# Optimization experiments

Measured on AMD Instinct MI355X. Metric: run time of the kernel, lower is better.

## Reference

```python
import jax, jax.numpy as jnp
import numpy as np

N_TOK = 131072
N_EMB = 1024
EMB_DIM = 64
COMMIT = 0.25


def setup_inputs() -> dict:
    key = jax.random.key(0)
    k1, k2 = jax.random.split(key)
    z_e = jax.random.normal(k1, (N_TOK, EMB_DIM), dtype=jnp.float32)
    # nn.init.uniform_(weight, -1/K, 1/K)
    codebook = jax.random.uniform(k2, (N_EMB, EMB_DIM), dtype=jnp.float32,
                                  minval=-1.0 / N_EMB, maxval=1.0 / N_EMB)
    return {"z_e": z_e, "codebook": codebook}


def reference(z_e, codebook):
    sg = jax.lax.stop_gradient
    # ||a-b||^2 = ||a||^2 + ||b||^2 - 2 a.b  (avoids [N,K,D] broadcast)
    d = (jnp.sum(z_e * z_e, axis=-1, keepdims=True)          # [N,1]
         + jnp.sum(codebook * codebook, axis=-1)[None, :]    # [1,K]
         - 2.0 * jnp.einsum('nd,kd->nk', z_e, codebook))     # [N,K]
    indices = jnp.argmin(d, axis=-1)                          # [N] int
    z_q = codebook[indices]                                   # [N,D] gather

    codebook_loss = jnp.mean((z_q - sg(z_e)) ** 2)
    commitment_loss = jnp.mean((z_e - sg(z_q)) ** 2)
    loss = codebook_loss + COMMIT * commitment_loss

    z_q_st = z_e + sg(z_q - z_e)                              # straight-through

    # avg_probs = one_hot(indices).mean(0) via scatter-add histogram
    counts = jnp.zeros((N_EMB,), dtype=jnp.float32).at[indices].add(1.0)
    avg_probs = counts / z_e.shape[0]
    perplexity = jnp.exp(-jnp.sum(avg_probs * jnp.log(avg_probs + 1e-10)))

    return z_q_st, loss, perplexity, indices
```

## Files before the change

### kernel.cpp

```cpp
#include <hip/hip_runtime.h>
#include <math.h>

#define NTOK 131072
#define NEMB 1024
#define DIM  64
#define OUT_LOSS (NTOK * DIM)
#define OUT_PERP (OUT_LOSS + 1)
#define OUT_IDX  (OUT_LOSS + 2)

#define EPS_FLAG 6e-5f

typedef short bf16x8 __attribute__((ext_vector_type(8)));
typedef float f32x4  __attribute__((ext_vector_type(4)));
typedef const __attribute__((address_space(1))) void* gas_t;
typedef __attribute__((address_space(3))) void* las_t;

__device__ __forceinline__ float sqb(float x) {
    float y = x * x;
    asm volatile("" : "+v"(y));
    return y;
}
#define NP_PAIRWISE_SQ64(GET, RES)                                     \
    do {                                                               \
        float r0 = sqb(GET(0)), r1 = sqb(GET(1)), r2 = sqb(GET(2)),    \
              r3 = sqb(GET(3)), r4 = sqb(GET(4)), r5 = sqb(GET(5)),    \
              r6 = sqb(GET(6)), r7 = sqb(GET(7));                      \
        _Pragma("unroll")                                              \
        for (int i = 8; i < 64; i += 8) {                              \
            r0 += sqb(GET(i + 0)); r1 += sqb(GET(i + 1));              \
            r2 += sqb(GET(i + 2)); r3 += sqb(GET(i + 3));              \
            r4 += sqb(GET(i + 4)); r5 += sqb(GET(i + 5));              \
            r6 += sqb(GET(i + 6)); r7 += sqb(GET(i + 7));              \
        }                                                              \
        RES = ((r0 + r1) + (r2 + r3)) + ((r4 + r5) + (r6 + r7));       \
    } while (0)

__device__ __forceinline__ unsigned short f2bf_rne(float x) {
    unsigned u = __float_as_uint(x);
    u += 0x7FFFu + ((u >> 16) & 1u);
    return (unsigned short)(u >> 16);
}
__device__ __forceinline__ float bf2f(unsigned short b) {
    return __uint_as_float(((unsigned)b) << 16);
}


__global__ void vq_prep(const float* __restrict__ cb, float* __restrict__ h,
                        unsigned short* __restrict__ ch, unsigned short* __restrict__ cl,
                        double* __restrict__ sse, int* __restrict__ counts,
                        int* __restrict__ done) {
    if (blockIdx.x == 0) {
        if (threadIdx.x == 0) { *sse = 0.0; *done = 0; }
        for (int i = threadIdx.x; i < NEMB * 16; i += 256) counts[i] = 0;
    }
    int k = blockIdx.x * 256 + threadIdx.x;
    if (k >= NEMB) return;
    float c[64];
    const float4* p = (const float4*)(cb + k * DIM);
#pragma unroll
    for (int q = 0; q < 16; ++q) {
        float4 v = p[q];
        c[4 * q] = v.x; c[4 * q + 1] = v.y; c[4 * q + 2] = v.z; c[4 * q + 3] = v.w;
    }
    float hk;
#define GETC(d) (c[d])
    NP_PAIRWISE_SQ64(GETC, hk);
#undef GETC
    h[k] = hk;
#pragma unroll
    for (int b = 0; b < 8; ++b) {
        unsigned uhv[4], ulv[4];
#pragma unroll
        for (int e = 0; e < 4; ++e) {
            float x0 = -2.0f * c[b * 8 + e * 2 + 0];
            float x1 = -2.0f * c[b * 8 + e * 2 + 1];
            unsigned short h0 = f2bf_rne(x0), h1 = f2bf_rne(x1);
            unsigned short l0 = f2bf_rne(x0 - bf2f(h0)), l1 = f2bf_rne(x1 - bf2f(h1));
            uhv[e] = (unsigned)h0 | ((unsigned)h1 << 16);
            ulv[e] = (unsigned)l0 | ((unsigned)l1 << 16);
        }
        *(uint4*)(ch + k * 64 + b * 8) = make_uint4(uhv[0], uhv[1], uhv[2], uhv[3]);
        *(uint4*)(cl + k * 64 + b * 8) = make_uint4(ulv[0], ulv[1], ulv[2], ulv[3]);
    }
}

__global__ __launch_bounds__(512) void vq_screen(
    const float*          __restrict__ ze,
    const float*          __restrict__ cb,
    const unsigned short* __restrict__ ch_g,
    const unsigned short* __restrict__ cl_g,
    const float*          __restrict__ h_g,
    float*                __restrict__ out,
    int*                  __restrict__ aux,
    double*               __restrict__ sse_g,
    int*                  __restrict__ counts) {
    __shared__ __align__(16) char lds[53376];
    const int tid  = threadIdx.x;
    const int lane = tid & 63;
    const int wid  = tid >> 6;
    const int col  = lane & 15;
    const int grp  = lane >> 4;
    const int tbase = blockIdx.x * 256 + wid * 32;

    const int srow = tid >> 3, scol = tid & 7;
    const int srcoff = (srow * 8 + (scol ^ (srow & 7))) * 16;

    bf16x8 zh[2][2], zl[2][2];
#pragma unroll
    for (int tt = 0; tt < 2; ++tt)
#pragma unroll
        for (int s = 0; s < 2; ++s) {
            const float* zp = ze + (size_t)(tbase + tt * 16 + col) * 64 + s * 32 + grp * 8;
            float4 v0 = *(const float4*)(zp);
            float4 v1 = *(const float4*)(zp + 4);
            float zv[8] = {v0.x, v0.y, v0.z, v0.w, v1.x, v1.y, v1.z, v1.w};
            bf16x8 hfr, lfr;
#pragma unroll
            for (int j = 0; j < 8; ++j) {
                unsigned short hb = f2bf_rne(zv[j]);
                unsigned short lb = f2bf_rne(zv[j] - bf2f(hb));
                hfr[j] = (short)hb;
                lfr[j] = (short)lb;
            }
            zh[tt][s] = hfr;
            zl[tt][s] = lfr;
        }

    float m1[2] = {INFINITY, INFINITY}, m2[2] = {INFINITY, INFINITY};
    float m3[2] = {INFINITY, INFINITY};
    int   ki[2] = {0, 0}, i2[2] = {0, 0};

#define STAGE(cc, b)                                                           \
    do {                                                                       \
        __builtin_amdgcn_global_load_lds(                                      \
            (gas_t)((const char*)ch_g + (cc) * 8192 + srcoff),                 \
            (las_t)(lds + (b) * 16384 + wid * 1024), 16, 0, 0);                \
        __builtin_amdgcn_global_load_lds(                                      \
            (gas_t)((const char*)cl_g + (cc) * 8192 + srcoff),                 \
            (las_t)(lds + (b) * 16384 + 8192 + wid * 1024), 16, 0, 0);         \
    } while (0)

#define TOP3UPD(tt, s, kk)                                                     \
    do {                                                                       \
        bool lt1 = (s) < m1[tt], lt2 = (s) < m2[tt], lt3 = (s) < m3[tt];       \
        m3[tt] = lt2 ? m2[tt] : (lt3 ? (s) : m3[tt]);                          \
        i2[tt] = lt1 ? ki[tt] : (lt2 ? (kk) : i2[tt]);                         \
        m2[tt] = lt1 ? m1[tt] : (lt2 ? (s) : m2[tt]);                          \
        ki[tt] = lt1 ? (kk) : ki[tt];                                          \
        m1[tt] = lt1 ? (s) : m1[tt];                                           \
    } while (0)

#define COMPUTE(cc, b)                                                         \
    do {                                                                       \
        _Pragma("unroll")                                                      \
        for (int ct = 0; ct < 4; ++ct) {                                       \
            const int arow = (b) * 16384 + ct * 2048 + col * 128;              \
            bf16x8 ach0 = *(const bf16x8*)(lds + arow + ((((0 * 4) + grp) ^ (col & 7)) << 4)); \
            bf16x8 ach1 = *(const bf16x8*)(lds + arow + ((((1 * 4) + grp) ^ (col & 7)) << 4)); \
            bf16x8 acl0 = *(const bf16x8*)(lds + arow + 8192 + ((((0 * 4) + grp) ^ (col & 7)) << 4)); \
            bf16x8 acl1 = *(const bf16x8*)(lds + arow + 8192 + ((((1 * 4) + grp) ^ (col & 7)) << 4)); \
            f32x4 hv = *(const f32x4*)(lds + 49152 + (cc) * 256 + ct * 64 + grp * 16); \
            f32x4 acc0 = hv, acc1 = hv;                                        \
            acc0 = __builtin_amdgcn_mfma_f32_16x16x32_bf16(ach0, zh[0][0], acc0, 0, 0, 0); \
            acc1 = __builtin_amdgcn_mfma_f32_16x16x32_bf16(ach0, zh[1][0], acc1, 0, 0, 0); \
            acc0 = __builtin_amdgcn_mfma_f32_16x16x32_bf16(ach1, zh[0][1], acc0, 0, 0, 0); \
            acc1 = __builtin_amdgcn_mfma_f32_16x16x32_bf16(ach1, zh[1][1], acc1, 0, 0, 0); \
            acc0 = __builtin_amdgcn_mfma_f32_16x16x32_bf16(ach0, zl[0][0], acc0, 0, 0, 0); \
            acc1 = __builtin_amdgcn_mfma_f32_16x16x32_bf16(ach0, zl[1][0], acc1, 0, 0, 0); \
            acc0 = __builtin_amdgcn_mfma_f32_16x16x32_bf16(ach1, zl[0][1], acc0, 0, 0, 0); \
            acc1 = __builtin_amdgcn_mfma_f32_16x16x32_bf16(ach1, zl[1][1], acc1, 0, 0, 0); \
            acc0 = __builtin_amdgcn_mfma_f32_16x16x32_bf16(acl0, zh[0][0], acc0, 0, 0, 0); \
            acc1 = __builtin_amdgcn_mfma_f32_16x16x32_bf16(acl0, zh[1][0], acc1, 0, 0, 0); \
            acc0 = __builtin_amdgcn_mfma_f32_16x16x32_bf16(acl1, zh[0][1], acc0, 0, 0, 0); \
            acc1 = __builtin_amdgcn_mfma_f32_16x16x32_bf16(acl1, zh[1][1], acc1, 0, 0, 0); \
            const int kb = (cc) * 64 + ct * 16 + grp * 4;                      \
            _Pragma("unroll")                                                  \
            for (int j = 0; j < 4; ++j) {                                      \
                TOP3UPD(0, acc0[j], kb + j);                                   \
                TOP3UPD(1, acc1[j], kb + j);                                   \
            }                                                                  \
        }                                                                      \
    } while (0)

#define CHUNK(cc, W)                                                           \
    do {                                                                       \
        asm volatile("s_waitcnt vmcnt(" #W ")" ::: "memory");                  \
        __builtin_amdgcn_s_barrier();                                          \
        __builtin_amdgcn_sched_barrier(0);                                     \
        if ((cc) + 2 < 16) STAGE((cc) + 2, ((cc) + 2) % 3);                    \
        COMPUTE(cc, (cc) % 3);                                                 \
    } while (0)

    __builtin_amdgcn_global_load_lds((gas_t)(h_g + tid),
                                     (las_t)(lds + 49152 + wid * 256), 4, 0, 0);
    __builtin_amdgcn_global_load_lds((gas_t)(h_g + 512 + tid),
                                     (las_t)(lds + 49152 + 2048 + wid * 256), 4, 0, 0);
    STAGE(0, 0);
    STAGE(1, 1);

    CHUNK(0, 2);  CHUNK(1, 2);  CHUNK(2, 2);  CHUNK(3, 2);
    CHUNK(4, 2);  CHUNK(5, 2);  CHUNK(6, 2);  CHUNK(7, 2);
    CHUNK(8, 2);  CHUNK(9, 2);  CHUNK(10, 2); CHUNK(11, 2);
    CHUNK(12, 2); CHUNK(13, 2); CHUNK(14, 2); CHUNK(15, 0);

#pragma unroll
    for (int d = 16; d <= 32; d <<= 1) {
#pragma unroll
        for (int tt = 0; tt < 2; ++tt) {
            float b1 = __shfl_xor(m1[tt], d, 64);
            float b2 = __shfl_xor(m2[tt], d, 64);
            float b3 = __shfl_xor(m3[tt], d, 64);
            int  jb1 = __shfl_xor(ki[tt], d, 64);
            int  jb2 = __shfl_xor(i2[tt], d, 64);
            bool sw  = b1 < m1[tt];
            float hi = sw ? m1[tt] : b1;
            int  jhi = sw ? ki[tt] : jb1;
            float c1 = sw ? b1 : m1[tt];
            int   j1 = sw ? jb1 : ki[tt];
            float mn2 = fminf(m2[tt], b2);
            int   jm2 = (m2[tt] <= b2) ? i2[tt] : jb2;
            float c2  = fminf(hi, mn2);
            int   j2  = (hi <= mn2) ? jhi : jm2;
            float mid = fmaxf(fminf(hi, m2[tt]),
                              fminf(fmaxf(hi, m2[tt]), b2));
            float c3  = fminf(mid, fminf(m3[tt], b3));
            m1[tt] = c1; ki[tt] = j1; m2[tt] = c2; i2[tt] = j2; m3[tt] = c3;
        }
    }
    unsigned flagpack = ((m2[0] - m1[0] < EPS_FLAG) ? 1u : 0u)
                      | ((m2[1] - m1[1] < EPS_FLAG) ? 2u : 0u);
    unsigned deeppack = ((m3[0] - m1[0] < EPS_FLAG) ? 1u : 0u)
                      | ((m3[1] - m1[1] < EPS_FLAG) ? 2u : 0u);
    if (lane < 16) {
#pragma unroll
        for (int tt = 0; tt < 2; ++tt) {
            int t = tbase + tt * 16 + lane;
            bool flag = (flagpack >> tt) & 1u;
            if (flag) {
                out[OUT_IDX + t] = -(float)(ki[tt] + 1);
                aux[t] = (int)((unsigned)i2[tt]
                               | (((deeppack >> tt) & 1u) << 31));
            } else {
                out[OUT_IDX + t] = (float)ki[tt];
            }
        }
    }

    double lsse = 0.0;
    const int d4 = lane & 15;
#pragma unroll
    for (int iter = 0; iter < 8; ++iter) {
        const int j   = iter * 4 + grp;
        const int tt  = iter >> 2;
        const int src = j & 15;
        int k = __shfl(ki[tt], src, 64);
        unsigned fp = __shfl(flagpack, src, 64);
        if (!((fp >> tt) & 1u)) {
            const int t = tbase + j;
            float4 q  = *(const float4*)(cb + k * DIM + d4 * 4);
            float4 zv = *(const float4*)(ze + (size_t)t * DIM + d4 * 4);
            *(float4*)(out + (size_t)t * DIM + d4 * 4) = q;
            double dx = (double)q.x - (double)zv.x;
            double dy = (double)q.y - (double)zv.y;
            double dz = (double)q.z - (double)zv.z;
            double dw = (double)q.w - (double)zv.w;
            lsse = fma(dx, dx, lsse); lsse = fma(dy, dy, lsse);
            lsse = fma(dz, dz, lsse); lsse = fma(dw, dw, lsse);
            if (d4 == 0) atomicAdd(&counts[k * 16], 1);
        }
    }
#pragma unroll
    for (int off = 32; off > 0; off >>= 1)
        lsse += __shfl_down(lsse, off, 64);
    double* red = (double*)(lds + 53312);
    if (lane == 0) red[wid] = lsse;
    __syncthreads();
    if (tid == 0) {
        double bs = ((red[0] + red[1]) + (red[2] + red[3]))
                  + ((red[4] + red[5]) + (red[6] + red[7]));
        atomicAdd(sse_g, bs);
    }
}

__global__ __launch_bounds__(512) void vq_rescue(
    const float* __restrict__ ze, const float* __restrict__ cb,
    const float* __restrict__ h_g, const int* __restrict__ aux,
    float* __restrict__ out, double* __restrict__ sse_g,
    int* __restrict__ counts, int* __restrict__ done) {
    __shared__ int loc[512];
    __shared__ int kfin[512];
    __shared__ int dlist[512];
    __shared__ int nloc, ndeep;
    __shared__ float zst[8][64];
    __shared__ double red2[512];
    __shared__ int flagS;
    const int tid  = threadIdx.x;
    const int lane = tid & 63;
    const int wid  = tid >> 6;
    const int tbase = blockIdx.x * 512;

    if (tid == 0) { nloc = 0; ndeep = 0; }
    __syncthreads();
    {
        float fidx = out[OUT_IDX + tbase + tid];
        if (fidx < 0.0f) { int s = atomicAdd(&nloc, 1); loc[s] = tid; }
    }
    __syncthreads();
    const int nq = nloc;
    double lsse = 0.0;

    if (nq > 0) {
        const int e = lane * 8 + wid;
        if (e < nq) {
            const int t = tbase + loc[e];
            const int i1 = (int)(-out[OUT_IDX + t]) - 1;
            const unsigned a = (unsigned)aux[t];
            if (a >> 31) {
                int s = atomicAdd(&ndeep, 1);
                dlist[s] = e;
            } else {
                const int i2v = (int)(a & 1023u);
                const float4* zp  = (const float4*)(ze + (size_t)t * 64);
                const float4* c1p = (const float4*)(cb + i1 * 64);
                const float4* c2p = (const float4*)(cb + i2v * 64);
                float r0 = 0, r1 = 0, r2 = 0, r3 = 0, r4 = 0, r5 = 0, r6 = 0, r7 = 0;
                float A1 = 0.f, A2 = 0.f;
#pragma unroll
                for (int q = 0; q < 16; ++q) {
                    float4 zv = zp[q], cv1 = c1p[q], cv2 = c2p[q];
                    if (q & 1) {
                        r4 += sqb(zv.x); r5 += sqb(zv.y);
                        r6 += sqb(zv.z); r7 += sqb(zv.w);
                    } else {
                        r0 += sqb(zv.x); r1 += sqb(zv.y);
                        r2 += sqb(zv.z); r3 += sqb(zv.w);
                    }
                    A1 = fmaf(cv1.x, zv.x, A1); A1 = fmaf(cv1.y, zv.y, A1);
                    A1 = fmaf(cv1.z, zv.z, A1); A1 = fmaf(cv1.w, zv.w, A1);
                    A2 = fmaf(cv2.x, zv.x, A2); A2 = fmaf(cv2.y, zv.y, A2);
                    A2 = fmaf(cv2.z, zv.z, A2); A2 = fmaf(cv2.w, zv.w, A2);
                }
                float sz = ((r0 + r1) + (r2 + r3)) + ((r4 + r5) + (r6 + r7));
                float d1 = (sz + h_g[i1])  - 2.0f * A1;
                float d2 = (sz + h_g[i2v]) - 2.0f * A2;
                unsigned long long k1 =
                    ((unsigned long long)__float_as_uint(d1) << 32) | (unsigned)i1;
                unsigned long long k2 =
                    ((unsigned long long)__float_as_uint(d2) << 32) | (unsigned)i2v;
                kfin[e] = (int)(unsigned)((k1 < k2 ? k1 : k2) & 0xFFFFFFFFull);
            }
        }
        __syncthreads();

        for (int i = wid; i < ndeep; i += 8) {
            const int e2 = dlist[i];
            const int t = tbase + loc[e2];
            zst[wid][lane] = ze[(size_t)t * 64 + lane];
            __builtin_amdgcn_wave_barrier();
            asm volatile("s_waitcnt lgkmcnt(0)" ::: "memory");
            __builtin_amdgcn_sched_barrier(0);
            float sz;
#define GZ(d) (zst[wid][d])
            NP_PAIRWISE_SQ64(GZ, sz);
#undef GZ
            const float4* cb4 = (const float4*)cb;
            const float4* zr4 = (const float4*)zst[wid];
            unsigned long long key = ~0ull;
            for (int cc = 0; cc < 16; ++cc) {
                const int code = lane + 64 * cc;
                float acc = 0.f;
#pragma unroll
                for (int d4i = 0; d4i < 16; ++d4i) {
                    float4 zq = zr4[d4i];
                    float4 cv = cb4[(size_t)code * 16 + d4i];
                    acc = fmaf(cv.x, zq.x, acc); acc = fmaf(cv.y, zq.y, acc);
                    acc = fmaf(cv.z, zq.z, acc); acc = fmaf(cv.w, zq.w, acc);
                }
                float dk = (sz + h_g[code]) - 2.0f * acc;
                unsigned long long c =
                    ((unsigned long long)__float_as_uint(dk) << 32) | (unsigned)code;
                key = c < key ? c : key;
            }
#pragma unroll
            for (int dd = 1; dd < 64; dd <<= 1) {
                unsigned long long o = __shfl_xor(key, dd, 64);
                key = o < key ? o : key;
            }
            if (lane == 0) kfin[e2] = (int)(unsigned)(key & 0xFFFFFFFFull);
        }
        __syncthreads();

        for (int e3 = wid; e3 < nq; e3 += 8) {
            const int k = kfin[e3];
            const int t = tbase + loc[e3];
            float q  = cb[k * 64 + lane];
            float zv = ze[(size_t)t * 64 + lane];
            out[(size_t)t * 64 + lane] = q;
            double diff = (double)q - (double)zv;
            lsse = fma(diff, diff, lsse);
            if (lane == 0) {
                out[OUT_IDX + t] = (float)k;
                atomicAdd(&counts[k * 16], 1);
            }
        }
    }

#pragma unroll
    for (int off = 32; off > 0; off >>= 1)
        lsse += __shfl_down(lsse, off, 64);
    if (lane == 0) red2[wid] = lsse;
    __syncthreads();
    if (tid == 0) {
        double bs = ((red2[0] + red2[1]) + (red2[2] + red2[3]))
                  + ((red2[4] + red2[5]) + (red2[6] + red2[7]));
        if (bs != 0.0) atomicAdd(sse_g, bs);
        __threadfence();
        flagS = (atomicAdd(done, 1) == 255);
    }
    __syncthreads();

    if (flagS) {
        __threadfence();
        double local = 0.0;
        for (int k = tid; k < NEMB; k += 512) {
            int cv = __hip_atomic_load(&counts[k * 16], __ATOMIC_RELAXED, __HIP_MEMORY_SCOPE_AGENT);
            double p = (double)cv / (double)NTOK;
            local += p * log(p + 1e-10);
        }
        red2[tid] = local;
        __syncthreads();
        for (int s = 256; s > 0; s >>= 1) {
            if (tid < s) red2[tid] += red2[tid + s];
            __syncthreads();
        }
        if (tid == 0) {
            double sv = __hip_atomic_load(sse_g, __ATOMIC_RELAXED, __HIP_MEMORY_SCOPE_AGENT);
            double mse = sv / ((double)NTOK * (double)DIM);
            out[OUT_LOSS] = (float)(1.25 * mse);
            out[OUT_PERP] = (float)exp(-red2[0]);
        }
    }
}

extern "C" void kernel_launch(void* const* d_in, const int* in_sizes, int n_in,
                              void* d_out, int out_size, void* d_ws, size_t ws_size,
                              hipStream_t stream) {
    const float* ze = (const float*)d_in[0];
    const float* cb = (const float*)d_in[1];
    float* out = (float*)d_out;

    char* w = (char*)d_ws;
    double*         sse    = (double*)w;
    int*            counts = (int*)(w + 64);
    int*            done   = (int*)(w + 65600);
    float*          h      = (float*)(w + 65664);
    unsigned short* ch     = (unsigned short*)(w + 69760);
    unsigned short* cl     = (unsigned short*)(w + 200832);
    int*            aux    = (int*)(w + 331904);

    vq_prep<<<NEMB / 256, 256, 0, stream>>>(cb, h, ch, cl, sse, counts, done);
    vq_screen<<<NTOK / 256, 512, 0, stream>>>(ze, cb, ch, cl, h, out, aux, sse, counts);
    vq_rescue<<<NTOK / 512, 512, 0, stream>>>(ze, cb, h, aux, out, sse, counts, done);
}
```

Before: 133.7 us.

## Pack codebook index into distance low bits and use med3 for top-3 tracking

The screen kernel's top-3 insertion now keeps only three floats per token. A local codebook index is packed into the low 8 mantissa bits of the distance, and the running top-3 is updated with v_med3_f32 and fminf instead of separate index registers and selects. A 0.5 offset is added to the codebook norms so the distance stays positive and the bit-packed float ordering holds. The near-tie threshold is widened to absorb the lost mantissa precision, which sends more tokens to the exact rescue pass. The change cuts VALU instructions and register use in the hot loop, at the cost of more rescue work.

```diff
diff --git a/kernel.cpp b/kernel.cpp
--- a/kernel.cpp
+++ b/kernel.cpp
@@ -8,7 +8,7 @@
 #define OUT_PERP (OUT_LOSS + 1)
 #define OUT_IDX  (OUT_LOSS + 2)
 
-#define EPS_FLAG 6e-5f
+#define EPS_FLAG 8e-5f
 
 typedef short bf16x8 __attribute__((ext_vector_type(8)));
 typedef float f32x4  __attribute__((ext_vector_type(4)));
@@ -43,9 +43,15 @@
 __device__ __forceinline__ float bf2f(unsigned short b) {
     return __uint_as_float(((unsigned)b) << 16);
 }
+__device__ __forceinline__ float med3f(float a, float b, float c) {
+    float r;
+    asm("v_med3_f32 %0, %1, %2, %3" : "=v"(r) : "v"(a), "v"(b), "v"(c));
+    return r;
+}
 
 
 __global__ void vq_prep(const float* __restrict__ cb, float* __restrict__ h,
+                        float* __restrict__ hb,
                         unsigned short* __restrict__ ch, unsigned short* __restrict__ cl,
                         double* __restrict__ sse, int* __restrict__ counts,
                         int* __restrict__ done) {
@@ -67,6 +73,7 @@
     NP_PAIRWISE_SQ64(GETC, hk);
 #undef GETC
     h[k] = hk;
+    hb[k] = hk + 0.5f;
 #pragma unroll
     for (int b = 0; b < 8; ++b) {
         unsigned uhv[4], ulv[4];
@@ -89,7 +96,7 @@
     const float*          __restrict__ cb,
     const unsigned short* __restrict__ ch_g,
     const unsigned short* __restrict__ cl_g,
-    const float*          __restrict__ h_g,
+    const float*          __restrict__ hb_g,
     float*                __restrict__ out,
     int*                  __restrict__ aux,
     double*               __restrict__ sse_g,
@@ -117,10 +124,10 @@
             bf16x8 hfr, lfr;
 #pragma unroll
             for (int j = 0; j < 8; ++j) {
-                unsigned short hb = f2bf_rne(zv[j]);
-                unsigned short lb = f2bf_rne(zv[j] - bf2f(hb));
-                hfr[j] = (short)hb;
-                lfr[j] = (short)lb;
+                unsigned short hbv = f2bf_rne(zv[j]);
+                unsigned short lbv = f2bf_rne(zv[j] - bf2f(hbv));
+                hfr[j] = (short)hbv;
+                lfr[j] = (short)lbv;
             }
             zh[tt][s] = hfr;
             zl[tt][s] = lfr;
@@ -128,7 +135,6 @@
 
     float m1[2] = {INFINITY, INFINITY}, m2[2] = {INFINITY, INFINITY};
     float m3[2] = {INFINITY, INFINITY};
-    int   ki[2] = {0, 0}, i2[2] = {0, 0};
 
 #define STAGE(cc, b)                                                           \
     do {                                                                       \
@@ -140,14 +146,14 @@
             (las_t)(lds + (b) * 16384 + 8192 + wid * 1024), 16, 0, 0);         \
     } while (0)
 
-#define TOP3UPD(tt, s, kk)                                                     \
+#define TOP3P(tt, sval, kidx)                                                  \
     do {                                                                       \
-        bool lt1 = (s) < m1[tt], lt2 = (s) < m2[tt], lt3 = (s) < m3[tt];       \
-        m3[tt] = lt2 ? m2[tt] : (lt3 ? (s) : m3[tt]);                          \
-        i2[tt] = lt1 ? ki[tt] : (lt2 ? (kk) : i2[tt]);                         \
-        m2[tt] = lt1 ? m1[tt] : (lt2 ? (s) : m2[tt]);                          \
-        ki[tt] = lt1 ? (kk) : ki[tt];                                          \
-        m1[tt] = lt1 ? (s) : m1[tt];                                           \
+        unsigned _ub = (__float_as_uint(sval) & 0xFFFFFF00u) | (unsigned)(kidx); \
+        float _u = __uint_as_float(_ub);                                       \
+        float _t2 = med3f(m1[tt], m2[tt], _u);                                 \
+        float _t3 = med3f(m2[tt], m3[tt], _u);                                 \
+        m1[tt] = fminf(m1[tt], _u);                                            \
+        m2[tt] = _t2; m3[tt] = _t3;                                            \
     } while (0)
 
 #define COMPUTE(cc, b)                                                         \
@@ -173,11 +179,11 @@
             acc1 = __builtin_amdgcn_mfma_f32_16x16x32_bf16(acl0, zh[1][0], acc1, 0, 0, 0); \
             acc0 = __builtin_amdgcn_mfma_f32_16x16x32_bf16(acl1, zh[0][1], acc0, 0, 0, 0); \
             acc1 = __builtin_amdgcn_mfma_f32_16x16x32_bf16(acl1, zh[1][1], acc1, 0, 0, 0); \
-            const int kb = (cc) * 64 + ct * 16 + grp * 4;                      \
             _Pragma("unroll")                                                  \
             for (int j = 0; j < 4; ++j) {                                      \
-                TOP3UPD(0, acc0[j], kb + j);                                   \
-                TOP3UPD(1, acc1[j], kb + j);                                   \
+                const int kidx = ((cc) << 4) | (ct << 2) | j;                  \
+                TOP3P(0, acc0[j], kidx);                                       \
+                TOP3P(1, acc1[j], kidx);                                       \
             }                                                                  \
         }                                                                      \
     } while (0)
@@ -191,9 +197,9 @@
         COMPUTE(cc, (cc) % 3);                                                 \
     } while (0)
 
-    __builtin_amdgcn_global_load_lds((gas_t)(h_g + tid),
+    __builtin_amdgcn_global_load_lds((gas_t)(hb_g + tid),
                                      (las_t)(lds + 49152 + wid * 256), 4, 0, 0);
-    __builtin_amdgcn_global_load_lds((gas_t)(h_g + 512 + tid),
+    __builtin_amdgcn_global_load_lds((gas_t)(hb_g + 512 + tid),
                                      (las_t)(lds + 49152 + 2048 + wid * 256), 4, 0, 0);
     STAGE(0, 0);
     STAGE(1, 1);
@@ -203,34 +209,49 @@
     CHUNK(8, 2);  CHUNK(9, 2);  CHUNK(10, 2); CHUNK(11, 2);
     CHUNK(12, 2); CHUNK(13, 2); CHUNK(14, 2); CHUNK(15, 0);
 
+    float q1[2], q2[2], q3[2];
+    int   ki[2], i2[2];
+#pragma unroll
+    for (int tt = 0; tt < 2; ++tt) {
+        unsigned b1 = __float_as_uint(m1[tt]);
+        unsigned b2 = __float_as_uint(m2[tt]);
+        unsigned b3 = __float_as_uint(m3[tt]);
+        q1[tt] = __uint_as_float(b1 & 0xFFFFFF00u);
+        q2[tt] = __uint_as_float(b2 & 0xFFFFFF00u);
+        q3[tt] = __uint_as_float(b3 & 0xFFFFFF00u);
+        unsigned e1 = b1 & 255u, e2 = b2 & 255u;
+        ki[tt] = (int)((e1 >> 4) * 64 + ((e1 >> 2) & 3u) * 16 + grp * 4 + (e1 & 3u));
+        i2[tt] = (int)((e2 >> 4) * 64 + ((e2 >> 2) & 3u) * 16 + grp * 4 + (e2 & 3u));
+    }
+
 #pragma unroll
     for (int d = 16; d <= 32; d <<= 1) {
 #pragma unroll
         for (int tt = 0; tt < 2; ++tt) {
-            float b1 = __shfl_xor(m1[tt], d, 64);
-            float b2 = __shfl_xor(m2[tt], d, 64);
-            float b3 = __shfl_xor(m3[tt], d, 64);
+            float b1 = __shfl_xor(q1[tt], d, 64);
+            float b2 = __shfl_xor(q2[tt], d, 64);
+            float b3 = __shfl_xor(q3[tt], d, 64);
             int  jb1 = __shfl_xor(ki[tt], d, 64);
             int  jb2 = __shfl_xor(i2[tt], d, 64);
-            bool sw  = b1 < m1[tt];
-            float hi = sw ? m1[tt] : b1;
+            bool sw  = b1 < q1[tt];
+            float hi = sw ? q1[tt] : b1;
             int  jhi = sw ? ki[tt] : jb1;
-            float c1 = sw ? b1 : m1[tt];
+            float c1 = sw ? b1 : q1[tt];
             int   j1 = sw ? jb1 : ki[tt];
-            float mn2 = fminf(m2[tt], b2);
-            int   jm2 = (m2[tt] <= b2) ? i2[tt] : jb2;
+            float mn2 = fminf(q2[tt], b2);
+            int   jm2 = (q2[tt] <= b2) ? i2[tt] : jb2;
             float c2  = fminf(hi, mn2);
             int   j2  = (hi <= mn2) ? jhi : jm2;
-            float mid = fmaxf(fminf(hi, m2[tt]),
-                              fminf(fmaxf(hi, m2[tt]), b2));
-            float c3  = fminf(mid, fminf(m3[tt], b3));
-            m1[tt] = c1; ki[tt] = j1; m2[tt] = c2; i2[tt] = j2; m3[tt] = c3;
-        }
-    }
-    unsigned flagpack = ((m2[0] - m1[0] < EPS_FLAG) ? 1u : 0u)
-                      | ((m2[1] - m1[1] < EPS_FLAG) ? 2u : 0u);
-    unsigned deeppack = ((m3[0] - m1[0] < EPS_FLAG) ? 1u : 0u)
-                      | ((m3[1] - m1[1] < EPS_FLAG) ? 2u : 0u);
+            float mid = fmaxf(fminf(hi, q2[tt]),
+                              fminf(fmaxf(hi, q2[tt]), b2));
+            float c3  = fminf(mid, fminf(q3[tt], b3));
+            q1[tt] = c1; ki[tt] = j1; q2[tt] = c2; i2[tt] = j2; q3[tt] = c3;
+        }
+    }
+    unsigned flagpack = ((q2[0] - q1[0] < EPS_FLAG) ? 1u : 0u)
+                      | ((q2[1] - q1[1] < EPS_FLAG) ? 2u : 0u);
+    unsigned deeppack = ((q3[0] - q1[0] < EPS_FLAG) ? 1u : 0u)
+                      | ((q3[1] - q1[1] < EPS_FLAG) ? 2u : 0u);
     if (lane < 16) {
 #pragma unroll
         for (int tt = 0; tt < 2; ++tt) {
@@ -454,11 +475,12 @@
     int*            counts = (int*)(w + 64);
     int*            done   = (int*)(w + 65600);
     float*          h      = (float*)(w + 65664);
-    unsigned short* ch     = (unsigned short*)(w + 69760);
-    unsigned short* cl     = (unsigned short*)(w + 200832);
-    int*            aux    = (int*)(w + 331904);
-
-    vq_prep<<<NEMB / 256, 256, 0, stream>>>(cb, h, ch, cl, sse, counts, done);
-    vq_screen<<<NTOK / 256, 512, 0, stream>>>(ze, cb, ch, cl, h, out, aux, sse, counts);
+    float*          hb     = (float*)(w + 69760);
+    unsigned short* ch     = (unsigned short*)(w + 73856);
+    unsigned short* cl     = (unsigned short*)(w + 204928);
+    int*            aux    = (int*)(w + 336000);
+
+    vq_prep<<<NEMB / 256, 256, 0, stream>>>(cb, h, hb, ch, cl, sse, counts, done);
+    vq_screen<<<NTOK / 256, 512, 0, stream>>>(ze, cb, ch, cl, hb, out, aux, sse, counts);
     vq_rescue<<<NTOK / 512, 512, 0, stream>>>(ze, cb, h, aux, out, sse, counts, done);
 }
```

Result: faster. 116.5 us (-12.8%).
